# Kernel tuning notes

Measured on AMD Instinct MI355X. Metric: run time of the kernel, lower is better.

The kernel has to match this reference:

```python
import jax, jax.numpy as jnp
import numpy as np

D = 192
HEADS = 4
HD = D // HEADS
R = 3  # correlation radius actually used in forward_level
NDISP = (2 * R + 1) ** 2  # 49
T = 3  # frames -> 2 consecutive pairs
ITERS = 4


def layer_norm(x, w, b, eps=1e-5):
    m = jnp.mean(x, axis=-1, keepdims=True)
    v = jnp.var(x, axis=-1, keepdims=True)
    return (x - m) / jnp.sqrt(v + eps) * w + b


def mha(x, in_w, in_b, out_w, out_b):
    # torch nn.MultiheadAttention, batch_first, self-attention
    B, N, _ = x.shape
    qkv = x @ in_w.T + in_b
    q, k, v = jnp.split(qkv, 3, axis=-1)
    q = q.reshape(B, N, HEADS, HD).transpose(0, 2, 1, 3) * (1.0 / float(np.sqrt(HD)))
    k = k.reshape(B, N, HEADS, HD).transpose(0, 2, 1, 3)
    v = v.reshape(B, N, HEADS, HD).transpose(0, 2, 1, 3)
    att = jax.nn.softmax(jnp.einsum('bhqd,bhkd->bhqk', q, k), axis=-1)
    y = jnp.einsum('bhqk,bhkd->bhqd', att, v).transpose(0, 2, 1, 3).reshape(B, N, D)
    return y @ out_w.T + out_b


def tblock(x, p):
    ln1w, ln1b, inw, inb, ow, ob, ln2w, ln2b, w1, b1, w2, b2 = p
    x = x + mha(layer_norm(x, ln1w, ln1b), inw, inb, ow, ob)
    h = layer_norm(x, ln2w, ln2b)
    h = jax.nn.gelu(h @ w1.T + b1, approximate=False) @ w2.T + b2
    return x + h


def local_corr(f1, f2):
    C = f1.shape[1]
    scale = 1.0 / float(np.sqrt(C))
    outs = []
    for dy in range(-R, R + 1):
        for dx in range(-R, R + 1):
            f2s = jnp.roll(f2, (dy, dx), axis=(2, 3))
            outs.append(jnp.sum(f1 * f2s, axis=1) * scale)
    return jnp.stack(outs, axis=1)


def grid_sample_bilinear_border(img, grid):
    # img: B,C,H,W; grid: B,Ho,Wo,2 with (x,y) in [-1,1]; align_corners=True, border padding
    B, C, H, W = img.shape
    x = jnp.clip((grid[..., 0] + 1.0) * 0.5 * (W - 1), 0.0, W - 1)
    y = jnp.clip((grid[..., 1] + 1.0) * 0.5 * (H - 1), 0.0, H - 1)
    x0 = jnp.floor(x); y0 = jnp.floor(y)
    x1 = jnp.minimum(x0 + 1, W - 1); y1 = jnp.minimum(y0 + 1, H - 1)
    wx = (x - x0)[:, None]; wy = (y - y0)[:, None]
    imgf = img.reshape(B, C, H * W)
    Ho, Wo = x.shape[1], x.shape[2]
    def gather(yy, xx):
        idx = (yy * W + xx).astype(jnp.int32).reshape(B, 1, Ho * Wo)
        return jnp.take_along_axis(imgf, idx, axis=2).reshape(B, C, Ho, Wo)
    v00 = gather(y0, x0); v01 = gather(y0, x1)
    v10 = gather(y1, x0); v11 = gather(y1, x1)
    return v00 * (1 - wx) * (1 - wy) + v01 * wx * (1 - wy) + v10 * (1 - wx) * wy + v11 * wx * wy


def warp(img, flow):
    # flow in pixels, Bx2xHxW
    B, C, H, W = img.shape
    xs = jnp.linspace(-1.0, 1.0, W); ys = jnp.linspace(-1.0, 1.0, H)
    gx, gy = jnp.meshgrid(xs, ys)  # each (H, W), 'xy' indexing
    base = jnp.stack([gx, gy], axis=-1)[None]
    off = jnp.stack([flow[:, 0] * (2.0 / max(W - 1, 1)),
                     flow[:, 1] * (2.0 / max(H - 1, 1))], axis=-1)
    return grid_sample_bilinear_border(img, base + off)


def upsample2x_align(img):
    # F.interpolate(scale_factor=2, mode='bilinear', align_corners=True)
    B, C, H, W = img.shape
    Ho, Wo = 2 * H, 2 * W
    xs = jnp.linspace(-1.0, 1.0, Wo); ys = jnp.linspace(-1.0, 1.0, Ho)
    gx, gy = jnp.meshgrid(xs, ys)
    grid = jnp.broadcast_to(jnp.stack([gx, gy], axis=-1)[None], (B, Ho, Wo, 2))
    return grid_sample_bilinear_border(img, grid)


def conv2d(x, w, b):
    y = jax.lax.conv_general_dilated(x, w, (1, 1), ((1, 1), (1, 1)),
                                     dimension_numbers=('NCHW', 'OIHW', 'NCHW'))
    return y + b[None, :, None, None]


def _forward(feats_l1, feats_l2, feats_l3, tok_w, tok_b,
             lcm_ln1_w, lcm_ln1_b, lcm_in_w, lcm_in_b, lcm_out_w, lcm_out_b,
             lcm_ln2_w, lcm_ln2_b, lcm_mlp_w1, lcm_mlp_b1, lcm_mlp_w2, lcm_mlp_b2,
             gtr_ln1_w, gtr_ln1_b, gtr_in_w, gtr_in_b, gtr_out_w, gtr_out_b,
             gtr_ln2_w, gtr_ln2_b, gtr_mlp_w1, gtr_mlp_b1, gtr_mlp_w2, gtr_mlp_b2,
             head_w1, head_b1, head_w2, head_b2,
             ref1_w1, ref1_b1, ref1_w2, ref1_b2,
             ref0_w1, ref0_b1, ref0_w2, ref0_b2):
    feats = [[feats_l1[t] for t in range(T)],
             [feats_l2[t] for t in range(T)],
             [feats_l3[t] for t in range(T)]]
    # ---- CostTokenizer ----
    tokens = []
    for lvl in range(3):
        toks = []
        for k in range(T - 1):
            corr = local_corr(feats[lvl][k], feats[lvl][k + 1])
            toks.append(jnp.einsum('bchw,dc->bdhw', corr, tok_w[lvl]) + tok_b[lvl][None, :, None, None])
        tokens.append(toks)
    lcm_p = [(lcm_ln1_w[i], lcm_ln1_b[i], lcm_in_w[i], lcm_in_b[i], lcm_out_w[i], lcm_out_b[i],
              lcm_ln2_w[i], lcm_ln2_b[i], lcm_mlp_w1[i], lcm_mlp_b1[i], lcm_mlp_w2[i], lcm_mlp_b2[i])
             for i in range(lcm_ln1_w.shape[0])]
    gtr_p = [(gtr_ln1_w[i], gtr_ln1_b[i], gtr_in_w[i], gtr_in_b[i], gtr_out_w[i], gtr_out_b[i],
              gtr_ln2_w[i], gtr_ln2_b[i], gtr_mlp_w1[i], gtr_mlp_b1[i], gtr_mlp_w2[i], gtr_mlp_b2[i])
             for i in range(gtr_ln1_w.shape[0])]
    # ---- LatentCostMemory (EMA state; .detach() -> stop_gradient; state resets when N changes) ----
    state = None
    latent = []
    for toks in tokens:
        lvl_lat = []
        for tok in toks:
            B_, Dd, H, W = tok.shape
            x = tok.reshape(B_, Dd, H * W).transpose(0, 2, 1)  # b (h w) d
            for p in lcm_p:
                x = tblock(x, p)
            if state is None or state.shape[1] != x.shape[1]:
                state = jax.lax.stop_gradient(x)
            x = 0.8 * x + 0.2 * state
            state = jax.lax.stop_gradient(x)
            lvl_lat.append(x.transpose(0, 2, 1))  # b d n
        latent.append(lvl_lat)
    H8, W8 = feats[1][0].shape[-2:]
    coarse = []
    for lat in latent[1]:
        x = lat.transpose(0, 2, 1)
        for p in gtr_p:
            x = tblock(x, p)
        fv = jax.nn.gelu(x @ head_w1.T + head_b1, approximate=False) @ head_w2.T + head_b2
        coarse.append(fv.transpose(0, 2, 1).reshape(-1, 2, H8, W8))
    # ---- MSRecurrentDecoder ----
    outs = []
    for k, f8 in enumerate(coarse):
        cur = f8
        for _ in range(ITERS):
            w10 = warp(feats[1][k + 1], cur)
            x = jnp.concatenate([feats[1][k], cur, w10], axis=1)
            cur = cur + conv2d(jax.nn.gelu(conv2d(x, ref1_w1, ref1_b1), approximate=False), ref1_w2, ref1_b2)
        cur2 = upsample2x_align(cur)
        for _ in range(ITERS):
            w10 = warp(feats[0][k + 1], cur2)
            x = jnp.concatenate([feats[0][k], cur2, w10], axis=1)
            cur2 = cur2 + conv2d(jax.nn.gelu(conv2d(x, ref0_w1, ref0_b1), approximate=False), ref0_w2, ref0_b2)
        outs.append(cur2)
    return jnp.stack(outs)  # [pairs, B, 2, H/4, W/4]


def setup_inputs():
    key = jax.random.key(0)
    ks = iter(jax.random.split(key, 64))
    def rn(shape, s=1.0):
        return jax.random.normal(next(ks), shape, dtype=jnp.float32) * s
    B = 1
    inp = {}
    inp['feats_l1'] = rn((T, B, 64, 64, 64))
    inp['feats_l2'] = rn((T, B, 128, 32, 32))
    inp['feats_l3'] = rn((T, B, 192, 16, 16))
    inp['tok_w'] = rn((3, D, NDISP), 0.02)
    inp['tok_b'] = rn((3, D), 0.02)
    for pre, n in (('lcm', 6), ('gtr', 2)):
        inp[pre + '_ln1_w'] = jnp.ones((n, D), jnp.float32)
        inp[pre + '_ln1_b'] = jnp.zeros((n, D), jnp.float32)
        inp[pre + '_in_w'] = rn((n, 3 * D, D), 0.02)
        inp[pre + '_in_b'] = rn((n, 3 * D), 0.02)
        inp[pre + '_out_w'] = rn((n, D, D), 0.02)
        inp[pre + '_out_b'] = rn((n, D), 0.02)
        inp[pre + '_ln2_w'] = jnp.ones((n, D), jnp.float32)
        inp[pre + '_ln2_b'] = jnp.zeros((n, D), jnp.float32)
        inp[pre + '_mlp_w1'] = rn((n, 4 * D, D), 0.02)
        inp[pre + '_mlp_b1'] = rn((n, 4 * D), 0.02)
        inp[pre + '_mlp_w2'] = rn((n, D, 4 * D), 0.02)
        inp[pre + '_mlp_b2'] = rn((n, D), 0.02)
    inp['head_w1'] = rn((D, D), 0.02); inp['head_b1'] = rn((D,), 0.02)
    inp['head_w2'] = rn((2, D), 0.02); inp['head_b2'] = rn((2,), 0.02)
    inp['ref1_w1'] = rn((128, 258, 3, 3), 0.02); inp['ref1_b1'] = rn((128,), 0.02)
    inp['ref1_w2'] = rn((2, 128, 3, 3), 0.02); inp['ref1_b2'] = rn((2,), 0.02)
    inp['ref0_w1'] = rn((64, 130, 3, 3), 0.02); inp['ref0_b1'] = rn((64,), 0.02)
    inp['ref0_w2'] = rn((2, 64, 3, 3), 0.02); inp['ref0_b2'] = rn((2,), 0.02)
    return inp


def reference(feats_l1, feats_l2, feats_l3, tok_w, tok_b,
              lcm_ln1_w, lcm_ln1_b, lcm_in_w, lcm_in_b, lcm_out_w, lcm_out_b,
              lcm_ln2_w, lcm_ln2_b, lcm_mlp_w1, lcm_mlp_b1, lcm_mlp_w2, lcm_mlp_b2,
              gtr_ln1_w, gtr_ln1_b, gtr_in_w, gtr_in_b, gtr_out_w, gtr_out_b,
              gtr_ln2_w, gtr_ln2_b, gtr_mlp_w1, gtr_mlp_b1, gtr_mlp_w2, gtr_mlp_b2,
              head_w1, head_b1, head_w2, head_b2,
              ref1_w1, ref1_b1, ref1_w2, ref1_b2,
              ref0_w1, ref0_b1, ref0_w2, ref0_b2):
    return _forward(feats_l1, feats_l2, feats_l3, tok_w, tok_b,
                    lcm_ln1_w, lcm_ln1_b, lcm_in_w, lcm_in_b, lcm_out_w, lcm_out_b,
                    lcm_ln2_w, lcm_ln2_b, lcm_mlp_w1, lcm_mlp_b1, lcm_mlp_w2, lcm_mlp_b2,
                    gtr_ln1_w, gtr_ln1_b, gtr_in_w, gtr_in_b, gtr_out_w, gtr_out_b,
                    gtr_ln2_w, gtr_ln2_b, gtr_mlp_w1, gtr_mlp_b1, gtr_mlp_w2, gtr_mlp_b2,
                    head_w1, head_b1, head_w2, head_b2,
                    ref1_w1, ref1_b1, ref1_w2, ref1_b2,
                    ref0_w1, ref0_b1, ref0_w2, ref0_b2)
```

## Files before the change

### kernel.cpp

```cpp
#include <hip/hip_runtime.h>
#include <hip/hip_bf16.h>

typedef __hip_bfloat16 bf16;
typedef short bf16x8 __attribute__((ext_vector_type(8)));
typedef float f32x4 __attribute__((ext_vector_type(4)));

#define DEV __device__ __forceinline__

DEV float bf2f(bf16 v) { return __bfloat162float(v); }
DEV bf16 f2bf(float v) { return __float2bfloat16(v); }
DEV unsigned short bfr(float f) {
  bf16 h = __float2bfloat16(f);
  return *reinterpret_cast<unsigned short*>(&h);
}
DEV float shf(unsigned short u) {
  unsigned int x = ((unsigned int)u) << 16;
  return *reinterpret_cast<float*>(&x);
}
DEV float gelu_exact(float x) { return 0.5f * x * (1.0f + erff(x * 0.70710678118654752f)); }

DEV float ldw(const void* p, long i, int isb) {
  return isb ? __bfloat162float(((const bf16*)p)[i]) : ((const float*)p)[i];
}

__global__ void k_detect(const unsigned short* __restrict__ u, int* __restrict__ flag) {
  __shared__ int bad;
  if (threadIdx.x == 0) bad = 0;
  __syncthreads();
  for (int i = threadIdx.x; i < 8192; i += 256) {
    int expo = (u[i] >> 7) & 0xFF;
    if (expo >= 138) atomicOr(&bad, 1);
  }
  __syncthreads();
  if (threadIdx.x == 0) *flag = bad ? 0 : 1;
}
__global__ void k_setone(int* p) { *p = 1; }

__global__ void k_cvt(const void* __restrict__ s, float* __restrict__ d, int n,
                      const int* __restrict__ fl) {
  int isb = *fl;
  int i = blockIdx.x * blockDim.x + threadIdx.x;
  if (i < n) d[i] = ldw(s, i, isb);
}

__global__ void k_zerosh(unsigned short* __restrict__ p, int n8) {
  int i = blockIdx.x * blockDim.x + threadIdx.x;
  if (i < n8) { uint4 z = {0, 0, 0, 0}; *(uint4*)(p + (long)i * 8) = z; }
}

__global__ void k_padtokw(const void* __restrict__ tw, bf16* __restrict__ dst,
                          const int* __restrict__ fl) {
  int isb = *fl;
  int i = blockIdx.x * blockDim.x + threadIdx.x;
  if (i >= 12288) return;
  int n = i >> 6, k = i & 63;
  float v = (k < 49) ? ldw(tw, 9408 + (long)n * 49 + k, isb) : 0.0f;
  dst[i] = f2bf(v);
}

__global__ void k_packw(const void* __restrict__ src, bf16* __restrict__ dst,
                        int OC, int C, int ICT, int NP, int ICP, int n,
                        const int* __restrict__ fl) {
  int isb = *fl;
  int i = blockIdx.x * blockDim.x + threadIdx.x;
  if (i >= n) return;
  int s = i / (NP * ICP);
  int r = i - s * NP * ICP;
  int oc = r / ICP, icp = r - oc * ICP;
  float v = 0.0f;
  if (oc < OC) {
    int ic = -1;
    if (icp < C) ic = icp;
    else if (icp < 2 * C) ic = icp - C + C + 2;
    else if (icp < 2 * C + 2) ic = icp - 2 * C + C;
    if (ic >= 0 && ic < ICT) v = ldw(src, ((long)oc * ICT + ic) * 9 + s, isb);
  }
  dst[i] = f2bf(v);
}

__global__ void k_trans_feats(const void* __restrict__ in, bf16* __restrict__ Fp,
                              int F, int C, int HW, const int* __restrict__ fl) {
  int isb = *fl;
  int cpg = C >> 3;
  int n = F * HW * cpg;
  int i = blockIdx.x * blockDim.x + threadIdx.x;
  if (i >= n) return;
  int p = i % HW;
  int rem = i / HW;
  int c8 = rem % cpg;
  int f = rem / cpg;
  long base = (long)f * C * HW + (long)(c8 * 8) * HW + p;
  union { unsigned short u[8]; uint4 v; } pk;
#pragma unroll
  for (int j = 0; j < 8; ++j) pk.u[j] = bfr(ldw(in, base + (long)j * HW, isb));
  *(uint4*)((unsigned short*)Fp + ((long)f * HW + p) * C + c8 * 8) = pk.v;
}

template <int C, int ICP, int NP, int WW, int LGW>
__global__ __launch_bounds__(64, 2) void k_conv1d(
    const bf16* __restrict__ Fp, const float* __restrict__ flow,
    const bf16* __restrict__ Wp, const float* __restrict__ bias,
    bf16* __restrict__ out) {
  constexpr int HH = WW, HW = WW * WW;
  constexpr int ACW = 18, APX = 54;
  constexpr int NK = ICP / 32;
  __shared__ unsigned short As[APX][40];
  __shared__ int pofs[APX];
  __shared__ int doff[APX][4];
  __shared__ float dwt[APX][4];
  __shared__ float ffl[APX][2];
  int ln = threadIdx.x;
  int quad = ln >> 4, l16 = ln & 15;
  int n0 = blockIdx.x * 16, m0 = blockIdx.y * 16, b = blockIdx.z;
  int py0 = m0 >> LGW, px0 = m0 & (WW - 1);
  const unsigned short* fcur = (const unsigned short*)Fp + (long)b * HW * C;
  const unsigned short* fnxt = (const unsigned short*)Fp + (long)(b + 1) * HW * C;
  const float* fl = flow + (long)b * 2 * HW;
  if (ln < APX) {
    int sr = ln / ACW, sc = ln - sr * ACW;
    int py = py0 + sr - 1, px = px0 + sc - 1;
    bool in = py >= 0 && py < HH && px >= 0 && px < WW;
    int p = in ? (py * WW + px) : 0;
    pofs[ln] = in ? p * C : -1;
    float fx = in ? fl[p] : 0.0f, fy = in ? fl[HW + p] : 0.0f;
    float x = fminf(fmaxf((float)px + fx, 0.0f), (float)(WW - 1));
    float y = fminf(fmaxf((float)py + fy, 0.0f), (float)(HH - 1));
    int x0 = (int)floorf(x), y0 = (int)floorf(y);
    int x1 = min(x0 + 1, WW - 1), y1 = min(y0 + 1, HH - 1);
    float wx = x - (float)x0, wy = y - (float)y0;
    dwt[ln][0] = in ? (1 - wx) * (1 - wy) : 0.0f;
    dwt[ln][1] = in ? wx * (1 - wy) : 0.0f;
    dwt[ln][2] = in ? (1 - wx) * wy : 0.0f;
    dwt[ln][3] = in ? wx * wy : 0.0f;
    doff[ln][0] = (y0 * WW + x0) * C; doff[ln][1] = (y0 * WW + x1) * C;
    doff[ln][2] = (y1 * WW + x0) * C; doff[ln][3] = (y1 * WW + x1) * C;
    ffl[ln][0] = in ? fx : 0.0f; ffl[ln][1] = in ? fy : 0.0f;
  }
  const unsigned short* wrow = (const unsigned short*)Wp + (long)(n0 + l16) * ICP + quad * 8;
  f32x4 ac0 = {}, ac1 = {}, ac2 = {};
  for (int kc = 0; kc < NK; ++kc) {
    int chb = kc * 32;
    if (chb < C) {
      uint4 arg[4];
#pragma unroll
      for (int j = 0; j < 4; ++j) {
        int idx = ln + j * 64;
        if (idx < APX * 4) {
          int ap = idx >> 2, c4 = idx & 3;
          int po = pofs[ap];
          uint4 z = {0, 0, 0, 0};
          arg[j] = (po >= 0) ? *(const uint4*)(fcur + po + chb + c4 * 8) : z;
        }
      }
#pragma unroll
      for (int j = 0; j < 4; ++j) {
        int idx = ln + j * 64;
        if (idx < APX * 4) {
          int ap = idx >> 2, c4 = idx & 3;
          *(uint4*)&As[ap][c4 * 8] = arg[j];
        }
      }
    } else if (chb < 2 * C) {
#pragma unroll
      for (int j = 0; j < 4; ++j) {
        int idx = ln + j * 64;
        if (idx < APX * 4) {
          int ap = idx >> 2, c4 = idx & 3;
          int c = chb - C + c4 * 8;
          uint4 v0 = *(const uint4*)(fnxt + doff[ap][0] + c);
          uint4 v1 = *(const uint4*)(fnxt + doff[ap][1] + c);
          uint4 v2 = *(const uint4*)(fnxt + doff[ap][2] + c);
          uint4 v3 = *(const uint4*)(fnxt + doff[ap][3] + c);
          float q0 = dwt[ap][0], q1 = dwt[ap][1], q2 = dwt[ap][2], q3 = dwt[ap][3];
          union { unsigned short u[8]; uint4 v; } a0 = {.v = v0}, a1 = {.v = v1},
                                                  a2 = {.v = v2}, a3 = {.v = v3}, o;
#pragma unroll
          for (int e = 0; e < 8; ++e)
            o.u[e] = bfr(shf(a0.u[e]) * q0 + shf(a1.u[e]) * q1 +
                         shf(a2.u[e]) * q2 + shf(a3.u[e]) * q3);
          *(uint4*)&As[ap][c4 * 8] = o.v;
        }
      }
    } else {
#pragma unroll
      for (int j = 0; j < 4; ++j) {
        int idx = ln + j * 64;
        if (idx < APX * 4) {
          int ap = idx >> 2, c4 = idx & 3;
          union { unsigned short u[8]; uint4 v; } o = { .v = {0, 0, 0, 0} };
          if (c4 == 0) { o.u[0] = bfr(ffl[ap][0]); o.u[1] = bfr(ffl[ap][1]); }
          *(uint4*)&As[ap][c4 * 8] = o.v;
        }
      }
    }
#pragma unroll
    for (int s = 0; s < 9; ++s) {
      int ky = s / 3, kx = s - ky * 3;
      bf16x8 af = *(const bf16x8*)&As[ky * ACW + l16 + kx][quad * 8];
      bf16x8 wf = *(const bf16x8*)(wrow + (long)s * NP * ICP + chb);
      if (s % 3 == 0)      ac0 = __builtin_amdgcn_mfma_f32_16x16x32_bf16(af, wf, ac0, 0, 0, 0);
      else if (s % 3 == 1) ac1 = __builtin_amdgcn_mfma_f32_16x16x32_bf16(af, wf, ac1, 0, 0, 0);
      else                 ac2 = __builtin_amdgcn_mfma_f32_16x16x32_bf16(af, wf, ac2, 0, 0, 0);
    }
  }
  int n = n0 + l16;
  float bv = bias[n];
  long rowbase = (long)b * (HH + 2) * (WW + 2) + (long)(py0 + 1) * (WW + 2);
#pragma unroll
  for (int r = 0; r < 4; ++r) {
    int px = px0 + quad * 4 + r;
    float v = gelu_exact(ac0[r] + ac1[r] + ac2[r] + bv);
    ((unsigned short*)out)[(rowbase + px + 1) * NP + n] = bfr(v);
  }
}

template <int C, int WW, int LGW>
__global__ __launch_bounds__(256) void k_conv2_dot(
    const bf16* __restrict__ mid, const bf16* __restrict__ Wq,
    const float* __restrict__ bias, float* __restrict__ cur) {
  constexpr int HH = WW;
  constexpr int HW = HH * WW;
  constexpr int Wp2 = WW + 2;
  constexpr int CPL = C / 64;
  int tid = threadIdx.x, wv = tid >> 6, ln = tid & 63;
  int gw = blockIdx.x * 4 + wv;
  int b = gw >> (2 * LGW);
  int p = gw & (HW - 1);
  int py = p >> LGW, px = p & (WW - 1);
  float r0 = cur[((long)b * 2 + 0) * HW + p];
  float r1 = cur[((long)b * 2 + 1) * HW + p];
  float b0 = bias[0], b1 = bias[1];
  const unsigned short* base = (const unsigned short*)mid +
      ((long)b * (HH + 2) * Wp2 + (long)py * Wp2 + px) * C + ln * CPL;
  const unsigned short* wb = (const unsigned short*)Wq + ln * CPL;
  float s0 = 0.0f, s1 = 0.0f;
#pragma unroll
  for (int t = 0; t < 9; ++t) {
    int dy = t / 3, dx = t - dy * 3;
    const unsigned short* ar = base + ((long)dy * Wp2 + dx) * C;
    const unsigned short* w0r = wb + (long)(t * 16 + 0) * C;
    const unsigned short* w1r = wb + (long)(t * 16 + 1) * C;
    if (CPL == 2) {
      unsigned int a = *(const unsigned int*)ar;
      unsigned int q0 = *(const unsigned int*)w0r;
      unsigned int q1 = *(const unsigned int*)w1r;
      float a0 = shf((unsigned short)a), a1 = shf((unsigned short)(a >> 16));
      s0 += a0 * shf((unsigned short)q0) + a1 * shf((unsigned short)(q0 >> 16));
      s1 += a0 * shf((unsigned short)q1) + a1 * shf((unsigned short)(q1 >> 16));
    } else {
      float a0 = shf(ar[0]);
      s0 += a0 * shf(w0r[0]);
      s1 += a0 * shf(w1r[0]);
    }
  }
#pragma unroll
  for (int o = 32; o; o >>= 1) { s0 += __shfl_xor(s0, o); s1 += __shfl_xor(s1, o); }
  if (ln == 0) {
    cur[((long)b * 2 + 0) * HW + p] = s0 + b0 + r0;
    cur[((long)b * 2 + 1) * HW + p] = s1 + b1 + r1;
  }
}

__global__ void k_corr(const bf16* __restrict__ Fp2, bf16* __restrict__ corrT) {
  __shared__ unsigned short f1r[128];
  int p = blockIdx.x;
  int b = blockIdx.y;
  int t = threadIdx.x;
  const unsigned short* f1 = (const unsigned short*)Fp2 + ((long)b * 1024 + p) * 128;
  if (t < 16) *(uint4*)&f1r[t * 8] = *(const uint4*)(f1 + t * 8);
  __syncthreads();
  long rowo = ((long)b * 1024 + p) * 64;
  if (t < 49) {
    int dy = t / 7 - 3, dx = t % 7 - 3;
    int h = p >> 5, w = p & 31;
    int p2 = (((h - dy) & 31) << 5) | ((w - dx) & 31);
    const unsigned short* f2 = (const unsigned short*)Fp2 + ((long)(b + 1) * 1024 + p2) * 128;
    float s = 0.0f;
    for (int c = 0; c < 128; c += 8) {
      union { unsigned short u[8]; uint4 v; } av = { .v = *(const uint4*)&f1r[c] };
      union { unsigned short u[8]; uint4 v; } bv = { .v = *(const uint4*)(f2 + c) };
#pragma unroll
      for (int j = 0; j < 8; ++j) s += shf(av.u[j]) * shf(bv.u[j]);
    }
    corrT[rowo + t] = f2bf(s * 0.08838834764831845f);
  } else {
    corrT[rowo + t] = f2bf(0.0f);
  }
}

template <int KT, int NTW, int ACT, bool HASRES, int AMODE, int OUTBF, int VT>
__global__ __launch_bounds__(64, 2) void k_gemm_w(
    const void* __restrict__ A, const void* __restrict__ W, long woff,
    const void* __restrict__ bias, long boff, const int* __restrict__ flb,
    const float* __restrict__ res, void* __restrict__ C,
    int N, const int* __restrict__ fl,
    const unsigned short* __restrict__ mop, const float* __restrict__ mml,
    bf16* __restrict__ vtout,
    const void* __restrict__ lnw, long lnwoff,
    const void* __restrict__ lnb, long lnboff) {
  constexpr int NK = KT / 32;
  int isb = *fl;
  int ln = threadIdx.x;
  int quad = ln >> 4, l16 = ln & 15;
  int m0 = blockIdx.y * 16, n0 = blockIdx.x * (16 * NTW);
  __shared__ unsigned short Als[(AMODE >= 2) ? 16 : 1][200];
  if constexpr (AMODE == 3) {
    int row = ln >> 2, j = ln & 3;
    const float* xr = (const float*)A + (long)(m0 + row) * 192 + j * 48;
    float av[48];
#pragma unroll
    for (int q = 0; q < 12; ++q) {
      float4 v = *(const float4*)(xr + q * 4);
      av[q * 4 + 0] = v.x; av[q * 4 + 1] = v.y;
      av[q * 4 + 2] = v.z; av[q * 4 + 3] = v.w;
    }
    float sum = 0.0f;
#pragma unroll
    for (int q = 0; q < 48; ++q) sum += av[q];
    sum += __shfl_xor(sum, 1);
    sum += __shfl_xor(sum, 2);
    float mean = sum * (1.0f / 192.0f);
    float vs = 0.0f;
#pragma unroll
    for (int q = 0; q < 48; ++q) { float d = av[q] - mean; vs += d * d; }
    vs += __shfl_xor(vs, 1);
    vs += __shfl_xor(vs, 2);
    float rstd = rsqrtf(vs * (1.0f / 192.0f) + 1e-5f);
#pragma unroll
    for (int g = 0; g < 6; ++g) {
      union { unsigned short u[8]; uint4 v; } pk;
#pragma unroll
      for (int e = 0; e < 8; ++e) {
        long k = j * 48 + g * 8 + e;
        float gg = ldw(lnw, lnwoff + k, isb);
        float bb = ldw(lnb, lnboff + k, isb);
        pk.u[e] = bfr((av[g * 8 + e] - mean) * rstd * gg + bb);
      }
      *(uint4*)&Als[row][j * 48 + g * 8] = pk.v;
    }
  } else if constexpr (AMODE == 2) {
    int row = ln >> 2, j = ln & 3;
    int m = m0 + row;
    int rr = m & 1023, bb = m >> 10;
    long idx[4];
    float ms[4], ls[4];
    float Ms = -1e30f;
#pragma unroll
    for (int s = 0; s < 4; ++s) {
      idx[s] = (((long)s * 2 + bb) * 4 + j) * 1024 + rr;
      ms[s] = mml[idx[s] * 2];
      ls[s] = mml[idx[s] * 2 + 1];
      Ms = fmaxf(Ms, ms[s]);
    }
    float e4[4], L = 0.0f;
#pragma unroll
    for (int s = 0; s < 4; ++s) { e4[s] = __expf(ms[s] - Ms); L += ls[s] * e4[s]; }
    float invL = 1.0f / L;
#pragma unroll
    for (int g = 0; g < 6; ++g) {
      union { unsigned short u[8]; uint4 v; } pk;
#pragma unroll
      for (int e2 = 0; e2 < 8; ++e2) {
        float o = 0.0f;
#pragma unroll
        for (int s = 0; s < 4; ++s) o += shf(mop[idx[s] * 48 + g * 8 + e2]) * e4[s];
        pk.u[e2] = bfr(o * invL);
      }
      *(uint4*)&Als[row][j * 48 + g * 8] = pk.v;
    }
  }
  f32x4 acc[NTW] = {};
  auto lda = [&](int kc) -> bf16x8 {
    if constexpr (AMODE >= 2) {
      return *(const bf16x8*)&Als[l16][kc * 32 + quad * 8];
    } else if constexpr (AMODE == 1) {
      return *(const bf16x8*)((const unsigned short*)A + (long)(m0 + l16) * KT + kc * 32 + quad * 8);
    } else {
      const float* ap = (const float*)A + (long)(m0 + l16) * KT + kc * 32 + quad * 8;
      float4 a0 = *(const float4*)ap;
      float4 a1 = *(const float4*)(ap + 4);
      union { unsigned short u[8]; bf16x8 v; } pk;
      pk.u[0] = bfr(a0.x); pk.u[1] = bfr(a0.y); pk.u[2] = bfr(a0.z); pk.u[3] = bfr(a0.w);
      pk.u[4] = bfr(a1.x); pk.u[5] = bfr(a1.y); pk.u[6] = bfr(a1.z); pk.u[7] = bfr(a1.w);
      return pk.v;
    }
  };
  if (isb) {
    const unsigned short* wb = (const unsigned short*)W + woff + (long)l16 * KT + quad * 8;
    for (int kc = 0; kc < NK; ++kc) {
      bf16x8 af = lda(kc);
#pragma unroll
      for (int nt = 0; nt < NTW; ++nt) {
        bf16x8 wf = *(const bf16x8*)(wb + (long)(n0 + nt * 16) * KT + kc * 32);
        acc[nt] = __builtin_amdgcn_mfma_f32_16x16x32_bf16(af, wf, acc[nt], 0, 0, 0);
      }
    }
  } else {
    const float* wb = (const float*)W + woff + (long)l16 * KT + quad * 8;
    for (int kc = 0; kc < NK; ++kc) {
      bf16x8 af = lda(kc);
#pragma unroll
      for (int nt = 0; nt < NTW; ++nt) {
        const float* wp = wb + (long)(n0 + nt * 16) * KT + kc * 32;
        float4 w0 = *(const float4*)wp;
        float4 w1 = *(const float4*)(wp + 4);
        union { unsigned short u[8]; bf16x8 v; } pk;
        pk.u[0] = bfr(w0.x); pk.u[1] = bfr(w0.y); pk.u[2] = bfr(w0.z); pk.u[3] = bfr(w0.w);
        pk.u[4] = bfr(w1.x); pk.u[5] = bfr(w1.y); pk.u[6] = bfr(w1.z); pk.u[7] = bfr(w1.w);
        acc[nt] = __builtin_amdgcn_mfma_f32_16x16x32_bf16(af, pk.v, acc[nt], 0, 0, 0);
      }
    }
  }
  int isbb = *flb;
#pragma unroll
  for (int nt = 0; nt < NTW; ++nt) {
    int n = n0 + nt * 16 + l16;
    float bv = ldw(bias, boff + n, isbb);
#pragma unroll
    for (int r = 0; r < 4; ++r) {
      int m = m0 + quad * 4 + r;
      float v = acc[nt][r] + bv;
      if (HASRES) v += res[(long)m * N + n];
      if (ACT == 1) v = gelu_exact(v);
      if (OUTBF) ((bf16*)C)[(long)m * N + n] = f2bf(v);
      else ((float*)C)[(long)m * N + n] = v;
      if constexpr (VT) {
        if (n >= 384) {
          int hh = (n - 384) / 48, dd = (n - 384) % 48;
          int row = m & 1023, bb = m >> 10;
          vtout[((long)(bb * 4 + hh) * 48 + dd) * 1024 + row] = f2bf(v);
        }
      }
    }
  }
}

__global__ __launch_bounds__(256) void k_head2(const float* __restrict__ A,
                                               const void* __restrict__ W,
                                               const void* __restrict__ bias,
                                               float* __restrict__ C,
                                               const int* __restrict__ fl) {
  int isb = *fl;
  int wv = threadIdx.x >> 6, ln = threadIdx.x & 63;
  int gw = blockIdx.x * 4 + wv;
  int m = gw >> 1, n = gw & 1;
  const float* a = A + (long)m * 192;
  float s = 0.0f;
#pragma unroll
  for (int q = 0; q < 3; ++q) {
    int j = ln + q * 64;
    s += a[j] * ldw(W, (long)n * 192 + j, isb);
  }
  for (int o = 32; o; o >>= 1) s += __shfl_xor(s, o);
  if (ln == 0) {
    int b = m >> 10, p = m & 1023;
    C[((long)b * 2 + n) * 1024 + p] = s + ldw(bias, n, isb);
  }
}

__global__ __launch_bounds__(256) void k_attn_mfma(const bf16* __restrict__ qkv,
                                                   const bf16* __restrict__ vt,
                                                   unsigned short* __restrict__ opart,
                                                   float* __restrict__ ml) {
  __shared__ unsigned short Qs[64][72];
  __shared__ unsigned short Ks[64][72];
  __shared__ unsigned short Vs[48][72];
  __shared__ unsigned short Ps[64][72];
  int tid = threadIdx.x;
  int wv = tid >> 6, ln = tid & 63, quad = ln >> 4, l16 = ln & 15;
  int h = blockIdx.y, b = blockIdx.z;
  int qt = blockIdx.x >> 2, s = blockIdx.x & 3;
  int q0 = qt * 64;
  const unsigned short* qp = (const unsigned short*)qkv + (long)b * 1024 * 576;
  const unsigned short* vp = (const unsigned short*)vt + ((long)(b * 4 + h) * 48) * 1024;
  for (int i = tid; i < 384; i += 256) {
    int r = i / 6, c = i % 6;
    *(uint4*)&Qs[r][c * 8] = *(const uint4*)(qp + (long)(q0 + r) * 576 + h * 48 + c * 8);
  }
  for (int i = tid; i < 128; i += 256) {
    int r = i >> 1, c = 6 + (i & 1);
    uint4 z = {0, 0, 0, 0};
    *(uint4*)&Qs[r][c * 8] = z;
  }
  float m[4] = {-1e30f, -1e30f, -1e30f, -1e30f};
  float l[4] = {0.0f, 0.0f, 0.0f, 0.0f};
  f32x4 accO[3] = {};
  const float SC = 0.14433756729740643f;
  for (int kc = s * 4; kc < s * 4 + 4; ++kc) {
    int k0 = kc * 64;
    for (int i = tid; i < 384; i += 256) {
      int r = i / 6, c = i % 6;
      *(uint4*)&Ks[r][c * 8] = *(const uint4*)(qp + (long)(k0 + r) * 576 + 192 + h * 48 + c * 8);
    }
    for (int i = tid; i < 128; i += 256) {
      int r = i >> 1, c = 6 + (i & 1);
      uint4 z = {0, 0, 0, 0};
      *(uint4*)&Ks[r][c * 8] = z;
    }
    for (int i = tid; i < 384; i += 256) {
      int d = i >> 3, c = i & 7;
      *(uint4*)&Vs[d][c * 8] = *(const uint4*)(vp + (long)d * 1024 + k0 + c * 8);
    }
    __syncthreads();
    f32x4 accS[4] = {};
    bf16x8 a0 = *(const bf16x8*)&Qs[wv * 16 + l16][quad * 8];
    bf16x8 a1 = *(const bf16x8*)&Qs[wv * 16 + l16][32 + quad * 8];
#pragma unroll
    for (int ct = 0; ct < 4; ++ct) {
      bf16x8 b0 = *(const bf16x8*)&Ks[ct * 16 + l16][quad * 8];
      bf16x8 b1 = *(const bf16x8*)&Ks[ct * 16 + l16][32 + quad * 8];
      accS[ct] = __builtin_amdgcn_mfma_f32_16x16x32_bf16(a0, b0, accS[ct], 0, 0, 0);
      accS[ct] = __builtin_amdgcn_mfma_f32_16x16x32_bf16(a1, b1, accS[ct], 0, 0, 0);
    }
#pragma unroll
    for (int r = 0; r < 4; ++r) {
      float s0 = accS[0][r] * SC, s1 = accS[1][r] * SC;
      float s2 = accS[2][r] * SC, s3 = accS[3][r] * SC;
      float mx = fmaxf(fmaxf(s0, s1), fmaxf(s2, s3));
      for (int o = 8; o; o >>= 1) mx = fmaxf(mx, __shfl_xor(mx, o));
      float mn = fmaxf(m[r], mx);
      float alpha = __expf(m[r] - mn);
      float p0 = __expf(s0 - mn), p1 = __expf(s1 - mn);
      float p2 = __expf(s2 - mn), p3 = __expf(s3 - mn);
      float rs = p0 + p1 + p2 + p3;
      for (int o = 8; o; o >>= 1) rs += __shfl_xor(rs, o);
      m[r] = mn;
      l[r] = l[r] * alpha + rs;
      accO[0][r] *= alpha; accO[1][r] *= alpha; accO[2][r] *= alpha;
      int prow = wv * 16 + quad * 4 + r;
      Ps[prow][l16]      = bfr(p0);
      Ps[prow][16 + l16] = bfr(p1);
      Ps[prow][32 + l16] = bfr(p2);
      Ps[prow][48 + l16] = bfr(p3);
    }
    bf16x8 pf0 = *(const bf16x8*)&Ps[wv * 16 + l16][quad * 8];
    bf16x8 pf1 = *(const bf16x8*)&Ps[wv * 16 + l16][32 + quad * 8];
#pragma unroll
    for (int ct = 0; ct < 3; ++ct) {
      bf16x8 v0 = *(const bf16x8*)&Vs[ct * 16 + l16][quad * 8];
      bf16x8 v1 = *(const bf16x8*)&Vs[ct * 16 + l16][32 + quad * 8];
      accO[ct] = __builtin_amdgcn_mfma_f32_16x16x32_bf16(pf0, v0, accO[ct], 0, 0, 0);
      accO[ct] = __builtin_amdgcn_mfma_f32_16x16x32_bf16(pf1, v1, accO[ct], 0, 0, 0);
    }
    __syncthreads();
  }
  long base = (((long)s * 2 + b) * 4 + h) * 1024;
#pragma unroll
  for (int r = 0; r < 4; ++r) {
    int row = q0 + wv * 16 + quad * 4 + r;
#pragma unroll
    for (int ct = 0; ct < 3; ++ct)
      opart[(base + row) * 48 + ct * 16 + l16] = bfr(accO[ct][r]);
    if (l16 == 0) {
      ml[(base + row) * 2]     = m[r];
      ml[(base + row) * 2 + 1] = l[r];
    }
  }
}

__global__ void k_ema(float* __restrict__ x) {
  int i = blockIdx.x * blockDim.x + threadIdx.x;
  if (i < 196608) x[196608 + i] = 0.8f * x[196608 + i] + 0.2f * x[i];
}

__global__ void k_upsample(const float* __restrict__ in, float* __restrict__ out) {
  int i = blockIdx.x * blockDim.x + threadIdx.x;
  if (i >= 2 * 2 * 64 * 64) return;
  int p = i & 4095;
  int bc = i >> 12;
  int oy = p >> 6, ox = p & 63;
  float sx = ox * (31.0f / 63.0f), sy = oy * (31.0f / 63.0f);
  int x0 = (int)sx, y0 = (int)sy;
  int x1 = min(x0 + 1, 31), y1 = min(y0 + 1, 31);
  float wx = sx - x0, wy = sy - y0;
  const float* ic = in + (long)bc * 1024;
  out[i] = ic[y0 * 32 + x0] * (1 - wx) * (1 - wy) + ic[y0 * 32 + x1] * wx * (1 - wy)
         + ic[y1 * 32 + x0] * (1 - wx) * wy      + ic[y1 * 32 + x1] * wx * wy;
}

__global__ void k_out(const float* __restrict__ cur2, void* __restrict__ out,
                      const int* __restrict__ fl) {
  int isb = *fl;
  int i = blockIdx.x * blockDim.x + threadIdx.x;
  if (i < 16384) {
    if (isb) ((bf16*)out)[i] = f2bf(cur2[i]);
    else ((float*)out)[i] = cur2[i];
  }
}

extern "C" void kernel_launch(void* const* d_in, const int* in_sizes, int n_in,
                              void* d_out, int out_size, void* d_ws, size_t ws_size,
                              hipStream_t stream) {
  const void* feats_l1 = d_in[0];
  const void* feats_l2 = d_in[1];
  const void* tok_w = d_in[3];
  const void* tok_b = d_in[4];
  const void* lcm_ln1_w = d_in[5];
  const void* lcm_ln1_b = d_in[6];
  const void* lcm_in_w  = d_in[7];
  const void* lcm_in_b  = d_in[8];
  const void* lcm_out_w = d_in[9];
  const void* lcm_out_b = d_in[10];
  const void* lcm_ln2_w = d_in[11];
  const void* lcm_ln2_b = d_in[12];
  const void* lcm_mlp_w1 = d_in[13];
  const void* lcm_mlp_b1 = d_in[14];
  const void* lcm_mlp_w2 = d_in[15];
  const void* lcm_mlp_b2 = d_in[16];
  const void* gtr_ln1_w = d_in[17];
  const void* gtr_ln1_b = d_in[18];
  const void* gtr_in_w  = d_in[19];
  const void* gtr_in_b  = d_in[20];
  const void* gtr_out_w = d_in[21];
  const void* gtr_out_b = d_in[22];
  const void* gtr_ln2_w = d_in[23];
  const void* gtr_ln2_b = d_in[24];
  const void* gtr_mlp_w1 = d_in[25];
  const void* gtr_mlp_b1 = d_in[26];
  const void* gtr_mlp_w2 = d_in[27];
  const void* gtr_mlp_b2 = d_in[28];
  const void* head_w1 = d_in[29];
  const void* head_b1 = d_in[30];
  const void* head_w2 = d_in[31];
  const void* head_b2 = d_in[32];
  const void* ref1_w1 = d_in[33];
  const void* ref1_b1 = d_in[34];
  const void* ref1_w2 = d_in[35];
  const void* ref1_b2 = d_in[36];
  const void* ref0_w1 = d_in[37];
  const void* ref0_b1 = d_in[38];
  const void* ref0_w2 = d_in[39];
  const void* ref0_b2 = d_in[40];
  (void)ws_size; (void)n_in; (void)in_sizes; (void)out_size;

  int* flag = (int*)d_ws;
  int* oneflag = (int*)d_ws + 2;
  float* wsf = (float*)d_ws;
  float* F2   = wsf + 16;
  float* rA   = F2 + 393216;
  float* rX   = rA + 786432;
  float* rT   = rX + 393216;
  float* rY   = rT + 393216;
  float* big  = rY + 393216;
  float* fv   = big + 1572864;
  float* cur  = fv + 4096;
  float* cur2 = cur + 4096;
  float* cb1a = cur2 + 16384;
  float* cb1b = cb1a + 128;
  float* cb0a = cb1b + 16;
  float* cb0b = cb0a + 64;
  bf16* wtok  = (bf16*)(cb0b + 16);
  float* wpk  = cb0b + 16 + 6144;
  bf16* w1p1 = (bf16*)wpk;
  bf16* w1p2 = (bf16*)(wpk + 165888);
  bf16* w0p1 = (bf16*)(wpk + 175104);
  bf16* w0p2 = (bf16*)(wpk + 221184);

  float* x = rX;
  bf16* corrTb = (bf16*)big;
  bf16* qkvbb  = (bf16*)big;
  bf16* vtb    = (bf16*)(big + 655360);
  bf16* hidb   = (bf16*)big;
  unsigned short* opart = (unsigned short*)rA;
  float* mlbuf = rY;
  float* headh = rT;
  bf16* mid0p = (bf16*)rT;
  bf16* mid1p = (bf16*)rY;
  bf16* Fp2   = (bf16*)(big + 851968);
  bf16* Fp1   = (bf16*)(big + 1048576);

  k_detect<<<1, 256, 0, stream>>>((const unsigned short*)feats_l1, flag);
  k_setone<<<1, 1, 0, stream>>>(oneflag);
  k_cvt<<<1, 256, 0, stream>>>(ref1_b1, cb1a, 128, flag);
  k_cvt<<<1, 256, 0, stream>>>(ref1_b2, cb1b, 2, flag);
  k_cvt<<<1, 256, 0, stream>>>(ref0_b1, cb0a, 64, flag);
  k_cvt<<<1, 256, 0, stream>>>(ref0_b2, cb0b, 2, flag);
  k_padtokw<<<48, 256, 0, stream>>>(tok_w, wtok, flag);
  k_packw<<<1296, 256, 0, stream>>>(ref1_w1, w1p1, 128, 128, 258, 128, 288, 331776, flag);
  k_packw<<<72, 256, 0, stream>>>(ref1_w2, w1p2, 2, 128, 128, 16, 128, 18432, flag);
  k_packw<<<360, 256, 0, stream>>>(ref0_w1, w0p1, 64, 64, 130, 64, 160, 92160, flag);
  k_packw<<<36, 256, 0, stream>>>(ref0_w2, w0p2, 2, 64, 64, 16, 64, 9216, flag);
  k_trans_feats<<<192, 256, 0, stream>>>(feats_l2, Fp2, 3, 128, 1024, flag);
  k_trans_feats<<<384, 256, 0, stream>>>(feats_l1, Fp1, 3, 64, 4096, flag);

  k_corr<<<dim3(1024, 2), 64, 0, stream>>>(Fp2, corrTb);
  k_gemm_w<64, 4, 0, false, 1, 0, 0><<<dim3(3, 128), 64, 0, stream>>>(
      corrTb, wtok, 0, tok_b, 192, flag, nullptr, x, 192, oneflag,
      nullptr, nullptr, nullptr, nullptr, 0, nullptr, 0);

  auto run_block = [&](const void* ln1w, long o1, const void* ln1b, long o2,
                       const void* inw, long o3, const void* inb, long o4,
                       const void* ow, long o5, const void* ob, long o6,
                       const void* ln2w, long o7, const void* ln2b, long o8,
                       const void* w1, long o9, const void* b1, long o10,
                       const void* w2, long o11, const void* b2, long o12) {
    k_gemm_w<192, 4, 0, false, 3, 1, 1><<<dim3(9, 128), 64, 0, stream>>>(
        x, inw, o3, inb, o4, flag, nullptr, qkvbb, 576, flag,
        nullptr, nullptr, vtb, ln1w, o1, ln1b, o2);
    k_attn_mfma<<<dim3(64, 4, 2), 256, 0, stream>>>(qkvbb, vtb, opart, mlbuf);
    k_gemm_w<192, 4, 0, true, 2, 0, 0><<<dim3(3, 128), 64, 0, stream>>>(
        nullptr, ow, o5, ob, o6, flag, x, x, 192, flag,
        opart, mlbuf, nullptr, nullptr, 0, nullptr, 0);
    k_gemm_w<192, 4, 1, false, 3, 1, 0><<<dim3(12, 128), 64, 0, stream>>>(
        x, w1, o9, b1, o10, flag, nullptr, hidb, 768, flag,
        nullptr, nullptr, nullptr, ln2w, o7, ln2b, o8);
    k_gemm_w<768, 4, 0, true, 1, 0, 0><<<dim3(3, 128), 64, 0, stream>>>(
        hidb, w2, o11, b2, o12, flag, x, x, 192, flag,
        nullptr, nullptr, nullptr, nullptr, 0, nullptr, 0);
  };

  for (int i = 0; i < 6; ++i) {
    run_block(lcm_ln1_w, (long)i * 192, lcm_ln1_b, (long)i * 192,
              lcm_in_w, (long)i * 110592, lcm_in_b, (long)i * 576,
              lcm_out_w, (long)i * 36864, lcm_out_b, (long)i * 192,
              lcm_ln2_w, (long)i * 192, lcm_ln2_b, (long)i * 192,
              lcm_mlp_w1, (long)i * 147456, lcm_mlp_b1, (long)i * 768,
              lcm_mlp_w2, (long)i * 147456, lcm_mlp_b2, (long)i * 192);
  }
  k_ema<<<768, 256, 0, stream>>>(x);

  for (int i = 0; i < 2; ++i) {
    run_block(gtr_ln1_w, (long)i * 192, gtr_ln1_b, (long)i * 192,
              gtr_in_w, (long)i * 110592, gtr_in_b, (long)i * 576,
              gtr_out_w, (long)i * 36864, gtr_out_b, (long)i * 192,
              gtr_ln2_w, (long)i * 192, gtr_ln2_b, (long)i * 192,
              gtr_mlp_w1, (long)i * 147456, gtr_mlp_b1, (long)i * 768,
              gtr_mlp_w2, (long)i * 147456, gtr_mlp_b2, (long)i * 192);
  }

  k_gemm_w<192, 4, 1, false, 0, 0, 0><<<dim3(3, 128), 64, 0, stream>>>(
      x, head_w1, 0, head_b1, 0, flag, nullptr, headh, 192, flag,
      nullptr, nullptr, nullptr, nullptr, 0, nullptr, 0);
  k_head2<<<1024, 256, 0, stream>>>(headh, head_w2, head_b2, cur, flag);

  k_zerosh<<<768, 256, 0, stream>>>((unsigned short*)rT, 196608);

  for (int it = 0; it < 4; ++it) {
    k_conv1d<128, 288, 128, 32, 5><<<dim3(8, 64, 2), 64, 0, stream>>>(
        Fp2, cur, w1p1, cb1a, mid1p);
    k_conv2_dot<128, 32, 5><<<512, 256, 0, stream>>>(mid1p, w1p2, cb1b, cur);
  }
  k_upsample<<<64, 256, 0, stream>>>(cur, cur2);

  for (int it = 0; it < 4; ++it) {
    k_conv1d<64, 160, 64, 64, 6><<<dim3(4, 256, 2), 64, 0, stream>>>(
        Fp1, cur2, w0p1, cb0a, mid0p);
    k_conv2_dot<64, 64, 6><<<2048, 256, 0, stream>>>(mid0p, w0p2, cb0b, cur2);
  }

  k_out<<<64, 256, 0, stream>>>(cur2, d_out, flag);
}
```

Baseline: 1.007 ms.

## Fuse transformer stack into persistent megakernel with software grid barriers

Replaces roughly 45 separate launches (token GEMM, 8 transformer blocks of 5 kernels each, EMA, and the head) with one persistent kernel of 256 blocks. The phases are separated by an atomic-counter grid barrier, and each wave walks the GEMM tiles in a grid-stride loop. The aim is to remove launch overhead and inter-kernel gaps between the many small GEMM and attention phases. In exchange, occupancy is capped at 256 blocks, and the spin barrier relies on all blocks being co-resident, which risks deadlock if they are not.

```diff
diff --git a/kernel.cpp b/kernel.cpp
--- a/kernel.cpp
+++ b/kernel.cpp
@@ -34,7 +34,7 @@
   __syncthreads();
   if (threadIdx.x == 0) *flag = bad ? 0 : 1;
 }
-__global__ void k_setone(int* p) { *p = 1; }
+__global__ void k_zero2(int* a, int* b) { *a = 0; *b = 0; }
 
 __global__ void k_cvt(const void* __restrict__ s, float* __restrict__ d, int n,
                       const int* __restrict__ fl) {
@@ -288,279 +288,351 @@
   }
 }
 
-template <int KT, int NTW, int ACT, bool HASRES, int AMODE, int OUTBF, int VT>
-__global__ __launch_bounds__(64, 2) void k_gemm_w(
-    const void* __restrict__ A, const void* __restrict__ W, long woff,
-    const void* __restrict__ bias, long boff, const int* __restrict__ flb,
-    const float* __restrict__ res, void* __restrict__ C,
-    int N, const int* __restrict__ fl,
-    const unsigned short* __restrict__ mop, const float* __restrict__ mml,
-    bf16* __restrict__ vtout,
-    const void* __restrict__ lnw, long lnwoff,
-    const void* __restrict__ lnb, long lnboff) {
+
+DEV void gridbar(int* cnt, int* gen) {
+  __threadfence();
+  __syncthreads();
+  if (threadIdx.x == 0) {
+    int g = atomicAdd(gen, 0);
+    if (atomicAdd(cnt, 1) == 255) {
+      atomicExch(cnt, 0);
+      atomicAdd(gen, 1);
+    } else {
+      while (atomicAdd(gen, 0) == g) __builtin_amdgcn_s_sleep(8);
+    }
+  }
+  __syncthreads();
+  __threadfence();
+}
+
+template <int KT, int ACT, bool HASRES, int AMODE, int OUTBF, int VT>
+DEV void gemm_ph(unsigned short* wls, int gw, int ln,
+                 const void* A, const void* W, long woff,
+                 const void* bias, long boff, int isbb,
+                 const float* res, void* C, int N, int isb,
+                 const unsigned short* mop, const float* mml, bf16* vtout,
+                 const void* lnw, long lnwoff, const void* lnb, long lnboff) {
   constexpr int NK = KT / 32;
-  int isb = *fl;
-  int ln = threadIdx.x;
   int quad = ln >> 4, l16 = ln & 15;
-  int m0 = blockIdx.y * 16, n0 = blockIdx.x * (16 * NTW);
-  __shared__ unsigned short Als[(AMODE >= 2) ? 16 : 1][200];
-  if constexpr (AMODE == 3) {
-    int row = ln >> 2, j = ln & 3;
-    const float* xr = (const float*)A + (long)(m0 + row) * 192 + j * 48;
-    float av[48];
-#pragma unroll
-    for (int q = 0; q < 12; ++q) {
-      float4 v = *(const float4*)(xr + q * 4);
-      av[q * 4 + 0] = v.x; av[q * 4 + 1] = v.y;
-      av[q * 4 + 2] = v.z; av[q * 4 + 3] = v.w;
-    }
-    float sum = 0.0f;
-#pragma unroll
-    for (int q = 0; q < 48; ++q) sum += av[q];
-    sum += __shfl_xor(sum, 1);
-    sum += __shfl_xor(sum, 2);
-    float mean = sum * (1.0f / 192.0f);
-    float vs = 0.0f;
-#pragma unroll
-    for (int q = 0; q < 48; ++q) { float d = av[q] - mean; vs += d * d; }
-    vs += __shfl_xor(vs, 1);
-    vs += __shfl_xor(vs, 2);
-    float rstd = rsqrtf(vs * (1.0f / 192.0f) + 1e-5f);
-#pragma unroll
-    for (int g = 0; g < 6; ++g) {
-      union { unsigned short u[8]; uint4 v; } pk;
-#pragma unroll
-      for (int e = 0; e < 8; ++e) {
-        long k = j * 48 + g * 8 + e;
-        float gg = ldw(lnw, lnwoff + k, isb);
-        float bb = ldw(lnb, lnboff + k, isb);
-        pk.u[e] = bfr((av[g * 8 + e] - mean) * rstd * gg + bb);
-      }
-      *(uint4*)&Als[row][j * 48 + g * 8] = pk.v;
-    }
-  } else if constexpr (AMODE == 2) {
-    int row = ln >> 2, j = ln & 3;
-    int m = m0 + row;
-    int rr = m & 1023, bb = m >> 10;
-    long idx[4];
-    float ms[4], ls[4];
-    float Ms = -1e30f;
-#pragma unroll
-    for (int s = 0; s < 4; ++s) {
-      idx[s] = (((long)s * 2 + bb) * 4 + j) * 1024 + rr;
-      ms[s] = mml[idx[s] * 2];
-      ls[s] = mml[idx[s] * 2 + 1];
-      Ms = fmaxf(Ms, ms[s]);
-    }
-    float e4[4], L = 0.0f;
-#pragma unroll
-    for (int s = 0; s < 4; ++s) { e4[s] = __expf(ms[s] - Ms); L += ls[s] * e4[s]; }
-    float invL = 1.0f / L;
-#pragma unroll
-    for (int g = 0; g < 6; ++g) {
-      union { unsigned short u[8]; uint4 v; } pk;
-#pragma unroll
-      for (int e2 = 0; e2 < 8; ++e2) {
-        float o = 0.0f;
-#pragma unroll
-        for (int s = 0; s < 4; ++s) o += shf(mop[idx[s] * 48 + g * 8 + e2]) * e4[s];
-        pk.u[e2] = bfr(o * invL);
-      }
-      *(uint4*)&Als[row][j * 48 + g * 8] = pk.v;
-    }
-  }
-  f32x4 acc[NTW] = {};
-  auto lda = [&](int kc) -> bf16x8 {
-    if constexpr (AMODE >= 2) {
-      return *(const bf16x8*)&Als[l16][kc * 32 + quad * 8];
-    } else if constexpr (AMODE == 1) {
-      return *(const bf16x8*)((const unsigned short*)A + (long)(m0 + l16) * KT + kc * 32 + quad * 8);
+  int ntn = N >> 6;
+  int ntiles = 128 * ntn;
+  for (int t = gw; t < ntiles; t += 1024) {
+    int tn = t % ntn, tm = t / ntn;
+    int m0 = tm * 16, n0 = tn * 64;
+    if constexpr (AMODE == 3) {
+      int row = ln >> 2, j = ln & 3;
+      const float* xr = (const float*)A + (long)(m0 + row) * 192 + j * 48;
+      float av[48];
+#pragma unroll
+      for (int q = 0; q < 12; ++q) {
+        float4 v = *(const float4*)(xr + q * 4);
+        av[q * 4 + 0] = v.x; av[q * 4 + 1] = v.y;
+        av[q * 4 + 2] = v.z; av[q * 4 + 3] = v.w;
+      }
+      float sum = 0.0f;
+#pragma unroll
+      for (int q = 0; q < 48; ++q) sum += av[q];
+      sum += __shfl_xor(sum, 1);
+      sum += __shfl_xor(sum, 2);
+      float mean = sum * (1.0f / 192.0f);
+      float vs = 0.0f;
+#pragma unroll
+      for (int q = 0; q < 48; ++q) { float d = av[q] - mean; vs += d * d; }
+      vs += __shfl_xor(vs, 1);
+      vs += __shfl_xor(vs, 2);
+      float rstd = rsqrtf(vs * (1.0f / 192.0f) + 1e-5f);
+#pragma unroll
+      for (int g = 0; g < 6; ++g) {
+        union { unsigned short u[8]; uint4 v; } pk;
+#pragma unroll
+        for (int e = 0; e < 8; ++e) {
+          long k = j * 48 + g * 8 + e;
+          float gg = ldw(lnw, lnwoff + k, isb);
+          float bb = ldw(lnb, lnboff + k, isb);
+          pk.u[e] = bfr((av[g * 8 + e] - mean) * rstd * gg + bb);
+        }
+        *(uint4*)&wls[row * 200 + j * 48 + g * 8] = pk.v;
+      }
+    } else if constexpr (AMODE == 2) {
+      int row = ln >> 2, j = ln & 3;
+      int m = m0 + row;
+      int rr = m & 1023, bb = m >> 10;
+      long idx[4];
+      float ms[4], ls[4];
+      float Ms = -1e30f;
+#pragma unroll
+      for (int s = 0; s < 4; ++s) {
+        idx[s] = (((long)s * 2 + bb) * 4 + j) * 1024 + rr;
+        ms[s] = mml[idx[s] * 2];
+        ls[s] = mml[idx[s] * 2 + 1];
+        Ms = fmaxf(Ms, ms[s]);
+      }
+      float e4[4], L = 0.0f;
+#pragma unroll
+      for (int s = 0; s < 4; ++s) { e4[s] = __expf(ms[s] - Ms); L += ls[s] * e4[s]; }
+      float invL = 1.0f / L;
+#pragma unroll
+      for (int g = 0; g < 6; ++g) {
+        union { unsigned short u[8]; uint4 v; } pk;
+#pragma unroll
+        for (int e2 = 0; e2 < 8; ++e2) {
+          float o = 0.0f;
+#pragma unroll
+          for (int s = 0; s < 4; ++s) o += shf(mop[idx[s] * 48 + g * 8 + e2]) * e4[s];
+          pk.u[e2] = bfr(o * invL);
+        }
+        *(uint4*)&wls[row * 200 + j * 48 + g * 8] = pk.v;
+      }
+    }
+    f32x4 acc[4] = {};
+    auto lda = [&](int kc) -> bf16x8 {
+      if constexpr (AMODE >= 2) {
+        return *(const bf16x8*)&wls[l16 * 200 + kc * 32 + quad * 8];
+      } else if constexpr (AMODE == 1) {
+        return *(const bf16x8*)((const unsigned short*)A + (long)(m0 + l16) * KT + kc * 32 + quad * 8);
+      } else {
+        const float* ap = (const float*)A + (long)(m0 + l16) * KT + kc * 32 + quad * 8;
+        float4 a0 = *(const float4*)ap;
+        float4 a1 = *(const float4*)(ap + 4);
+        union { unsigned short u[8]; bf16x8 v; } pk;
+        pk.u[0] = bfr(a0.x); pk.u[1] = bfr(a0.y); pk.u[2] = bfr(a0.z); pk.u[3] = bfr(a0.w);
+        pk.u[4] = bfr(a1.x); pk.u[5] = bfr(a1.y); pk.u[6] = bfr(a1.z); pk.u[7] = bfr(a1.w);
+        return pk.v;
+      }
+    };
+    if (isb) {
+      const unsigned short* wb = (const unsigned short*)W + woff + (long)l16 * KT + quad * 8;
+      for (int kc = 0; kc < NK; ++kc) {
+        bf16x8 af = lda(kc);
+#pragma unroll
+        for (int nt = 0; nt < 4; ++nt) {
+          bf16x8 wf = *(const bf16x8*)(wb + (long)(n0 + nt * 16) * KT + kc * 32);
+          acc[nt] = __builtin_amdgcn_mfma_f32_16x16x32_bf16(af, wf, acc[nt], 0, 0, 0);
+        }
+      }
     } else {
-      const float* ap = (const float*)A + (long)(m0 + l16) * KT + kc * 32 + quad * 8;
-      float4 a0 = *(const float4*)ap;
-      float4 a1 = *(const float4*)(ap + 4);
-      union { unsigned short u[8]; bf16x8 v; } pk;
-      pk.u[0] = bfr(a0.x); pk.u[1] = bfr(a0.y); pk.u[2] = bfr(a0.z); pk.u[3] = bfr(a0.w);
-      pk.u[4] = bfr(a1.x); pk.u[5] = bfr(a1.y); pk.u[6] = bfr(a1.z); pk.u[7] = bfr(a1.w);
-      return pk.v;
-    }
-  };
-  if (isb) {
-    const unsigned short* wb = (const unsigned short*)W + woff + (long)l16 * KT + quad * 8;
-    for (int kc = 0; kc < NK; ++kc) {
-      bf16x8 af = lda(kc);
-#pragma unroll
-      for (int nt = 0; nt < NTW; ++nt) {
-        bf16x8 wf = *(const bf16x8*)(wb + (long)(n0 + nt * 16) * KT + kc * 32);
-        acc[nt] = __builtin_amdgcn_mfma_f32_16x16x32_bf16(af, wf, acc[nt], 0, 0, 0);
-      }
-    }
-  } else {
-    const float* wb = (const float*)W + woff + (long)l16 * KT + quad * 8;
-    for (int kc = 0; kc < NK; ++kc) {
-      bf16x8 af = lda(kc);
-#pragma unroll
-      for (int nt = 0; nt < NTW; ++nt) {
-        const float* wp = wb + (long)(n0 + nt * 16) * KT + kc * 32;
-        float4 w0 = *(const float4*)wp;
-        float4 w1 = *(const float4*)(wp + 4);
-        union { unsigned short u[8]; bf16x8 v; } pk;
-        pk.u[0] = bfr(w0.x); pk.u[1] = bfr(w0.y); pk.u[2] = bfr(w0.z); pk.u[3] = bfr(w0.w);
-        pk.u[4] = bfr(w1.x); pk.u[5] = bfr(w1.y); pk.u[6] = bfr(w1.z); pk.u[7] = bfr(w1.w);
-        acc[nt] = __builtin_amdgcn_mfma_f32_16x16x32_bf16(af, pk.v, acc[nt], 0, 0, 0);
-      }
-    }
-  }
-  int isbb = *flb;
-#pragma unroll
-  for (int nt = 0; nt < NTW; ++nt) {
-    int n = n0 + nt * 16 + l16;
-    float bv = ldw(bias, boff + n, isbb);
-#pragma unroll
-    for (int r = 0; r < 4; ++r) {
-      int m = m0 + quad * 4 + r;
-      float v = acc[nt][r] + bv;
-      if (HASRES) v += res[(long)m * N + n];
-      if (ACT == 1) v = gelu_exact(v);
-      if (OUTBF) ((bf16*)C)[(long)m * N + n] = f2bf(v);
-      else ((float*)C)[(long)m * N + n] = v;
-      if constexpr (VT) {
-        if (n >= 384) {
-          int hh = (n - 384) / 48, dd = (n - 384) % 48;
-          int row = m & 1023, bb = m >> 10;
-          vtout[((long)(bb * 4 + hh) * 48 + dd) * 1024 + row] = f2bf(v);
-        }
-      }
-    }
-  }
-}
-
-__global__ __launch_bounds__(256) void k_head2(const float* __restrict__ A,
-                                               const void* __restrict__ W,
-                                               const void* __restrict__ bias,
-                                               float* __restrict__ C,
-                                               const int* __restrict__ fl) {
-  int isb = *fl;
-  int wv = threadIdx.x >> 6, ln = threadIdx.x & 63;
-  int gw = blockIdx.x * 4 + wv;
-  int m = gw >> 1, n = gw & 1;
-  const float* a = A + (long)m * 192;
-  float s = 0.0f;
-#pragma unroll
-  for (int q = 0; q < 3; ++q) {
-    int j = ln + q * 64;
-    s += a[j] * ldw(W, (long)n * 192 + j, isb);
-  }
-  for (int o = 32; o; o >>= 1) s += __shfl_xor(s, o);
-  if (ln == 0) {
-    int b = m >> 10, p = m & 1023;
-    C[((long)b * 2 + n) * 1024 + p] = s + ldw(bias, n, isb);
-  }
-}
-
-__global__ __launch_bounds__(256) void k_attn_mfma(const bf16* __restrict__ qkv,
-                                                   const bf16* __restrict__ vt,
-                                                   unsigned short* __restrict__ opart,
-                                                   float* __restrict__ ml) {
-  __shared__ unsigned short Qs[64][72];
-  __shared__ unsigned short Ks[64][72];
-  __shared__ unsigned short Vs[48][72];
-  __shared__ unsigned short Ps[64][72];
-  int tid = threadIdx.x;
+      const float* wb = (const float*)W + woff + (long)l16 * KT + quad * 8;
+      for (int kc = 0; kc < NK; ++kc) {
+        bf16x8 af = lda(kc);
+#pragma unroll
+        for (int nt = 0; nt < 4; ++nt) {
+          const float* wp = wb + (long)(n0 + nt * 16) * KT + kc * 32;
+          float4 w0 = *(const float4*)wp;
+          float4 w1 = *(const float4*)(wp + 4);
+          union { unsigned short u[8]; bf16x8 v; } pk;
+          pk.u[0] = bfr(w0.x); pk.u[1] = bfr(w0.y); pk.u[2] = bfr(w0.z); pk.u[3] = bfr(w0.w);
+          pk.u[4] = bfr(w1.x); pk.u[5] = bfr(w1.y); pk.u[6] = bfr(w1.z); pk.u[7] = bfr(w1.w);
+          acc[nt] = __builtin_amdgcn_mfma_f32_16x16x32_bf16(af, pk.v, acc[nt], 0, 0, 0);
+        }
+      }
+    }
+#pragma unroll
+    for (int nt = 0; nt < 4; ++nt) {
+      int n = n0 + nt * 16 + l16;
+      float bv = ldw(bias, boff + n, isbb);
+#pragma unroll
+      for (int r = 0; r < 4; ++r) {
+        int m = m0 + quad * 4 + r;
+        float v = acc[nt][r] + bv;
+        if (HASRES) v += res[(long)m * N + n];
+        if (ACT == 1) v = gelu_exact(v);
+        if (OUTBF) ((bf16*)C)[(long)m * N + n] = f2bf(v);
+        else ((float*)C)[(long)m * N + n] = v;
+        if constexpr (VT) {
+          if (n >= 384) {
+            int hh = (n - 384) / 48, dd = (n - 384) % 48;
+            int row = m & 1023, bb = m >> 10;
+            vtout[((long)(bb * 4 + hh) * 48 + dd) * 1024 + row] = f2bf(v);
+          }
+        }
+      }
+    }
+  }
+}
+
+DEV void attn_ph(unsigned short* SM, int bid, int tid,
+                 const bf16* qkv, const bf16* vt,
+                 unsigned short* opart, float* ml) {
+  unsigned short* Qs = SM;
+  unsigned short* Ks = SM + 64 * 72;
+  unsigned short* Vs = SM + 128 * 72;
+  unsigned short* Ps = SM + 176 * 72;
   int wv = tid >> 6, ln = tid & 63, quad = ln >> 4, l16 = ln & 15;
-  int h = blockIdx.y, b = blockIdx.z;
-  int qt = blockIdx.x >> 2, s = blockIdx.x & 3;
-  int q0 = qt * 64;
-  const unsigned short* qp = (const unsigned short*)qkv + (long)b * 1024 * 576;
-  const unsigned short* vp = (const unsigned short*)vt + ((long)(b * 4 + h) * 48) * 1024;
-  for (int i = tid; i < 384; i += 256) {
-    int r = i / 6, c = i % 6;
-    *(uint4*)&Qs[r][c * 8] = *(const uint4*)(qp + (long)(q0 + r) * 576 + h * 48 + c * 8);
-  }
-  for (int i = tid; i < 128; i += 256) {
-    int r = i >> 1, c = 6 + (i & 1);
-    uint4 z = {0, 0, 0, 0};
-    *(uint4*)&Qs[r][c * 8] = z;
-  }
-  float m[4] = {-1e30f, -1e30f, -1e30f, -1e30f};
-  float l[4] = {0.0f, 0.0f, 0.0f, 0.0f};
-  f32x4 accO[3] = {};
   const float SC = 0.14433756729740643f;
-  for (int kc = s * 4; kc < s * 4 + 4; ++kc) {
-    int k0 = kc * 64;
+  for (int u = bid; u < 512; u += 256) {
+    int bx = u & 63;
+    int h = (u >> 6) & 3, b = u >> 8;
+    int qt = bx >> 2, s = bx & 3;
+    int q0 = qt * 64;
+    const unsigned short* qp = (const unsigned short*)qkv + (long)b * 1024 * 576;
+    const unsigned short* vp = (const unsigned short*)vt + ((long)(b * 4 + h) * 48) * 1024;
     for (int i = tid; i < 384; i += 256) {
       int r = i / 6, c = i % 6;
-      *(uint4*)&Ks[r][c * 8] = *(const uint4*)(qp + (long)(k0 + r) * 576 + 192 + h * 48 + c * 8);
+      *(uint4*)&Qs[r * 72 + c * 8] = *(const uint4*)(qp + (long)(q0 + r) * 576 + h * 48 + c * 8);
     }
     for (int i = tid; i < 128; i += 256) {
       int r = i >> 1, c = 6 + (i & 1);
       uint4 z = {0, 0, 0, 0};
-      *(uint4*)&Ks[r][c * 8] = z;
-    }
-    for (int i = tid; i < 384; i += 256) {
-      int d = i >> 3, c = i & 7;
-      *(uint4*)&Vs[d][c * 8] = *(const uint4*)(vp + (long)d * 1024 + k0 + c * 8);
-    }
-    __syncthreads();
-    f32x4 accS[4] = {};
-    bf16x8 a0 = *(const bf16x8*)&Qs[wv * 16 + l16][quad * 8];
-    bf16x8 a1 = *(const bf16x8*)&Qs[wv * 16 + l16][32 + quad * 8];
-#pragma unroll
-    for (int ct = 0; ct < 4; ++ct) {
-      bf16x8 b0 = *(const bf16x8*)&Ks[ct * 16 + l16][quad * 8];
-      bf16x8 b1 = *(const bf16x8*)&Ks[ct * 16 + l16][32 + quad * 8];
-      accS[ct] = __builtin_amdgcn_mfma_f32_16x16x32_bf16(a0, b0, accS[ct], 0, 0, 0);
-      accS[ct] = __builtin_amdgcn_mfma_f32_16x16x32_bf16(a1, b1, accS[ct], 0, 0, 0);
-    }
+      *(uint4*)&Qs[r * 72 + c * 8] = z;
+    }
+    float m[4] = {-1e30f, -1e30f, -1e30f, -1e30f};
+    float l[4] = {0.0f, 0.0f, 0.0f, 0.0f};
+    f32x4 accO[3] = {};
+    for (int kc = s * 4; kc < s * 4 + 4; ++kc) {
+      int k0 = kc * 64;
+      for (int i = tid; i < 384; i += 256) {
+        int r = i / 6, c = i % 6;
+        *(uint4*)&Ks[r * 72 + c * 8] =
+            *(const uint4*)(qp + (long)(k0 + r) * 576 + 192 + h * 48 + c * 8);
+      }
+      for (int i = tid; i < 128; i += 256) {
+        int r = i >> 1, c = 6 + (i & 1);
+        uint4 z = {0, 0, 0, 0};
+        *(uint4*)&Ks[r * 72 + c * 8] = z;
+      }
+      for (int i = tid; i < 384; i += 256) {
+        int d = i >> 3, c = i & 7;
+        *(uint4*)&Vs[d * 72 + c * 8] = *(const uint4*)(vp + (long)d * 1024 + k0 + c * 8);
+      }
+      __syncthreads();
+      f32x4 accS[4] = {};
+      bf16x8 a0 = *(const bf16x8*)&Qs[(wv * 16 + l16) * 72 + quad * 8];
+      bf16x8 a1 = *(const bf16x8*)&Qs[(wv * 16 + l16) * 72 + 32 + quad * 8];
+#pragma unroll
+      for (int ct = 0; ct < 4; ++ct) {
+        bf16x8 b0 = *(const bf16x8*)&Ks[(ct * 16 + l16) * 72 + quad * 8];
+        bf16x8 b1 = *(const bf16x8*)&Ks[(ct * 16 + l16) * 72 + 32 + quad * 8];
+        accS[ct] = __builtin_amdgcn_mfma_f32_16x16x32_bf16(a0, b0, accS[ct], 0, 0, 0);
+        accS[ct] = __builtin_amdgcn_mfma_f32_16x16x32_bf16(a1, b1, accS[ct], 0, 0, 0);
+      }
+#pragma unroll
+      for (int r = 0; r < 4; ++r) {
+        float s0 = accS[0][r] * SC, s1 = accS[1][r] * SC;
+        float s2 = accS[2][r] * SC, s3 = accS[3][r] * SC;
+        float mx = fmaxf(fmaxf(s0, s1), fmaxf(s2, s3));
+        for (int o = 8; o; o >>= 1) mx = fmaxf(mx, __shfl_xor(mx, o));
+        float mn = fmaxf(m[r], mx);
+        float alpha = __expf(m[r] - mn);
+        float p0 = __expf(s0 - mn), p1 = __expf(s1 - mn);
+        float p2 = __expf(s2 - mn), p3 = __expf(s3 - mn);
+        float rs = p0 + p1 + p2 + p3;
+        for (int o = 8; o; o >>= 1) rs += __shfl_xor(rs, o);
+        m[r] = mn;
+        l[r] = l[r] * alpha + rs;
+        accO[0][r] *= alpha; accO[1][r] *= alpha; accO[2][r] *= alpha;
+        int prow = wv * 16 + quad * 4 + r;
+        Ps[prow * 72 + l16]      = bfr(p0);
+        Ps[prow * 72 + 16 + l16] = bfr(p1);
+        Ps[prow * 72 + 32 + l16] = bfr(p2);
+        Ps[prow * 72 + 48 + l16] = bfr(p3);
+      }
+      bf16x8 pf0 = *(const bf16x8*)&Ps[(wv * 16 + l16) * 72 + quad * 8];
+      bf16x8 pf1 = *(const bf16x8*)&Ps[(wv * 16 + l16) * 72 + 32 + quad * 8];
+#pragma unroll
+      for (int ct = 0; ct < 3; ++ct) {
+        bf16x8 v0 = *(const bf16x8*)&Vs[(ct * 16 + l16) * 72 + quad * 8];
+        bf16x8 v1 = *(const bf16x8*)&Vs[(ct * 16 + l16) * 72 + 32 + quad * 8];
+        accO[ct] = __builtin_amdgcn_mfma_f32_16x16x32_bf16(pf0, v0, accO[ct], 0, 0, 0);
+        accO[ct] = __builtin_amdgcn_mfma_f32_16x16x32_bf16(pf1, v1, accO[ct], 0, 0, 0);
+      }
+      __syncthreads();
+    }
+    long base = (((long)s * 2 + b) * 4 + h) * 1024;
 #pragma unroll
     for (int r = 0; r < 4; ++r) {
-      float s0 = accS[0][r] * SC, s1 = accS[1][r] * SC;
-      float s2 = accS[2][r] * SC, s3 = accS[3][r] * SC;
-      float mx = fmaxf(fmaxf(s0, s1), fmaxf(s2, s3));
-      for (int o = 8; o; o >>= 1) mx = fmaxf(mx, __shfl_xor(mx, o));
-      float mn = fmaxf(m[r], mx);
-      float alpha = __expf(m[r] - mn);
-      float p0 = __expf(s0 - mn), p1 = __expf(s1 - mn);
-      float p2 = __expf(s2 - mn), p3 = __expf(s3 - mn);
-      float rs = p0 + p1 + p2 + p3;
-      for (int o = 8; o; o >>= 1) rs += __shfl_xor(rs, o);
-      m[r] = mn;
-      l[r] = l[r] * alpha + rs;
-      accO[0][r] *= alpha; accO[1][r] *= alpha; accO[2][r] *= alpha;
-      int prow = wv * 16 + quad * 4 + r;
-      Ps[prow][l16]      = bfr(p0);
-      Ps[prow][16 + l16] = bfr(p1);
-      Ps[prow][32 + l16] = bfr(p2);
-      Ps[prow][48 + l16] = bfr(p3);
-    }
-    bf16x8 pf0 = *(const bf16x8*)&Ps[wv * 16 + l16][quad * 8];
-    bf16x8 pf1 = *(const bf16x8*)&Ps[wv * 16 + l16][32 + quad * 8];
-#pragma unroll
-    for (int ct = 0; ct < 3; ++ct) {
-      bf16x8 v0 = *(const bf16x8*)&Vs[ct * 16 + l16][quad * 8];
-      bf16x8 v1 = *(const bf16x8*)&Vs[ct * 16 + l16][32 + quad * 8];
-      accO[ct] = __builtin_amdgcn_mfma_f32_16x16x32_bf16(pf0, v0, accO[ct], 0, 0, 0);
-      accO[ct] = __builtin_amdgcn_mfma_f32_16x16x32_bf16(pf1, v1, accO[ct], 0, 0, 0);
-    }
-    __syncthreads();
-  }
-  long base = (((long)s * 2 + b) * 4 + h) * 1024;
-#pragma unroll
-  for (int r = 0; r < 4; ++r) {
-    int row = q0 + wv * 16 + quad * 4 + r;
-#pragma unroll
-    for (int ct = 0; ct < 3; ++ct)
-      opart[(base + row) * 48 + ct * 16 + l16] = bfr(accO[ct][r]);
-    if (l16 == 0) {
-      ml[(base + row) * 2]     = m[r];
-      ml[(base + row) * 2 + 1] = l[r];
-    }
-  }
-}
-
-__global__ void k_ema(float* __restrict__ x) {
-  int i = blockIdx.x * blockDim.x + threadIdx.x;
-  if (i < 196608) x[196608 + i] = 0.8f * x[196608 + i] + 0.2f * x[i];
+      int row = q0 + wv * 16 + quad * 4 + r;
+#pragma unroll
+      for (int ct = 0; ct < 3; ++ct)
+        opart[(base + row) * 48 + ct * 16 + l16] = bfr(accO[ct][r]);
+      if (l16 == 0) {
+        ml[(base + row) * 2]     = m[r];
+        ml[(base + row) * 2 + 1] = l[r];
+      }
+    }
+  }
+}
+
+__global__ __launch_bounds__(256, 2) void k_mega(
+    const int* flag, int* barcnt, int* bargen,
+    float* x, const bf16* corrTb, const bf16* wtok, const void* tok_b,
+    bf16* qkvbb, bf16* vtb, unsigned short* opart, float* mlbuf,
+    bf16* hidb, float* headh, float* cur,
+    const void* lcm_ln1_w, const void* lcm_ln1_b, const void* lcm_in_w, const void* lcm_in_b,
+    const void* lcm_out_w, const void* lcm_out_b, const void* lcm_ln2_w, const void* lcm_ln2_b,
+    const void* lcm_mlp_w1, const void* lcm_mlp_b1, const void* lcm_mlp_w2, const void* lcm_mlp_b2,
+    const void* gtr_ln1_w, const void* gtr_ln1_b, const void* gtr_in_w, const void* gtr_in_b,
+    const void* gtr_out_w, const void* gtr_out_b, const void* gtr_ln2_w, const void* gtr_ln2_b,
+    const void* gtr_mlp_w1, const void* gtr_mlp_b1, const void* gtr_mlp_w2, const void* gtr_mlp_b2,
+    const void* head_w1, const void* head_b1, const void* head_w2, const void* head_b2) {
+  __shared__ unsigned short SM[17280];
+  int tid = threadIdx.x, bid = blockIdx.x;
+  int wv = tid >> 6, ln = tid & 63;
+  int gw = bid * 4 + wv;
+  unsigned short* wls = SM + wv * 3200;
+  int isb = *flag;
+  gemm_ph<64, 0, false, 1, 0, 0>(wls, gw, ln, corrTb, wtok, 0, tok_b, 192, isb,
+                                 nullptr, x, 192, 1, nullptr, nullptr, nullptr,
+                                 nullptr, 0, nullptr, 0);
+  gridbar(barcnt, bargen);
+  for (int blk = 0; blk < 8; ++blk) {
+    long i = (blk < 6) ? blk : (blk - 6);
+    const void *ln1w, *ln1b, *inw, *inb, *ow, *ob, *ln2w, *ln2b, *w1, *b1, *w2, *b2;
+    if (blk < 6) {
+      ln1w = lcm_ln1_w; ln1b = lcm_ln1_b; inw = lcm_in_w; inb = lcm_in_b;
+      ow = lcm_out_w; ob = lcm_out_b; ln2w = lcm_ln2_w; ln2b = lcm_ln2_b;
+      w1 = lcm_mlp_w1; b1 = lcm_mlp_b1; w2 = lcm_mlp_w2; b2 = lcm_mlp_b2;
+    } else {
+      ln1w = gtr_ln1_w; ln1b = gtr_ln1_b; inw = gtr_in_w; inb = gtr_in_b;
+      ow = gtr_out_w; ob = gtr_out_b; ln2w = gtr_ln2_w; ln2b = gtr_ln2_b;
+      w1 = gtr_mlp_w1; b1 = gtr_mlp_b1; w2 = gtr_mlp_w2; b2 = gtr_mlp_b2;
+    }
+    long o1 = i * 192, o2 = i * 192, o3 = i * 110592, o4 = i * 576;
+    long o5 = i * 36864, o6 = i * 192, o7 = i * 192, o8 = i * 192;
+    long o9 = i * 147456, o10 = i * 768, o11 = i * 147456, o12 = i * 192;
+    gemm_ph<192, 0, false, 3, 1, 1>(wls, gw, ln, x, inw, o3, inb, o4, isb,
+                                    nullptr, qkvbb, 576, isb, nullptr, nullptr, vtb,
+                                    ln1w, o1, ln1b, o2);
+    gridbar(barcnt, bargen);
+    attn_ph(SM, bid, tid, qkvbb, vtb, opart, mlbuf);
+    gridbar(barcnt, bargen);
+    gemm_ph<192, 0, true, 2, 0, 0>(wls, gw, ln, nullptr, ow, o5, ob, o6, isb,
+                                   x, x, 192, isb, opart, mlbuf, nullptr,
+                                   nullptr, 0, nullptr, 0);
+    gridbar(barcnt, bargen);
+    gemm_ph<192, 1, false, 3, 1, 0>(wls, gw, ln, x, w1, o9, b1, o10, isb,
+                                    nullptr, hidb, 768, isb, nullptr, nullptr, nullptr,
+                                    ln2w, o7, ln2b, o8);
+    gridbar(barcnt, bargen);
+    gemm_ph<768, 0, true, 1, 0, 0>(wls, gw, ln, hidb, w2, o11, b2, o12, isb,
+                                   x, x, 192, isb, nullptr, nullptr, nullptr,
+                                   nullptr, 0, nullptr, 0);
+    gridbar(barcnt, bargen);
+    if (blk == 5) {
+      int gt = bid * 256 + tid;
+      for (int e = gt; e < 196608; e += 65536)
+        x[196608 + e] = 0.8f * x[196608 + e] + 0.2f * x[e];
+      gridbar(barcnt, bargen);
+    }
+  }
+  gemm_ph<192, 1, false, 0, 0, 0>(wls, gw, ln, x, head_w1, 0, head_b1, 0, isb,
+                                  nullptr, headh, 192, isb, nullptr, nullptr, nullptr,
+                                  nullptr, 0, nullptr, 0);
+  gridbar(barcnt, bargen);
+  for (int t2 = gw; t2 < 4096; t2 += 1024) {
+    int m = t2 >> 1, n = t2 & 1;
+    const float* a = headh + (long)m * 192;
+    float s = 0.0f;
+#pragma unroll
+    for (int q = 0; q < 3; ++q) {
+      int j = ln + q * 64;
+      s += a[j] * ldw(head_w2, (long)n * 192 + j, isb);
+    }
+    for (int o = 32; o; o >>= 1) s += __shfl_xor(s, o);
+    if (ln == 0) {
+      int b = m >> 10, p = m & 1023;
+      cur[((long)b * 2 + n) * 1024 + p] = s + ldw(head_b2, n, isb);
+    }
+  }
 }
 
 __global__ void k_upsample(const float* __restrict__ in, float* __restrict__ out) {
@@ -634,7 +706,8 @@
   (void)ws_size; (void)n_in; (void)in_sizes; (void)out_size;
 
   int* flag = (int*)d_ws;
-  int* oneflag = (int*)d_ws + 2;
+  int* barcnt = (int*)d_ws + 4;
+  int* bargen = (int*)d_ws + 5;
   float* wsf = (float*)d_ws;
   float* F2   = wsf + 16;
   float* rA   = F2 + 393216;
@@ -670,7 +743,7 @@
   bf16* Fp1   = (bf16*)(big + 1048576);
 
   k_detect<<<1, 256, 0, stream>>>((const unsigned short*)feats_l1, flag);
-  k_setone<<<1, 1, 0, stream>>>(oneflag);
+  k_zero2<<<1, 1, 0, stream>>>(barcnt, bargen);
   k_cvt<<<1, 256, 0, stream>>>(ref1_b1, cb1a, 128, flag);
   k_cvt<<<1, 256, 0, stream>>>(ref1_b2, cb1b, 2, flag);
   k_cvt<<<1, 256, 0, stream>>>(ref0_b1, cb0a, 64, flag);
@@ -684,54 +757,15 @@
   k_trans_feats<<<384, 256, 0, stream>>>(feats_l1, Fp1, 3, 64, 4096, flag);
 
   k_corr<<<dim3(1024, 2), 64, 0, stream>>>(Fp2, corrTb);
-  k_gemm_w<64, 4, 0, false, 1, 0, 0><<<dim3(3, 128), 64, 0, stream>>>(
-      corrTb, wtok, 0, tok_b, 192, flag, nullptr, x, 192, oneflag,
-      nullptr, nullptr, nullptr, nullptr, 0, nullptr, 0);
-
-  auto run_block = [&](const void* ln1w, long o1, const void* ln1b, long o2,
-                       const void* inw, long o3, const void* inb, long o4,
-                       const void* ow, long o5, const void* ob, long o6,
-                       const void* ln2w, long o7, const void* ln2b, long o8,
-                       const void* w1, long o9, const void* b1, long o10,
-                       const void* w2, long o11, const void* b2, long o12) {
-    k_gemm_w<192, 4, 0, false, 3, 1, 1><<<dim3(9, 128), 64, 0, stream>>>(
-        x, inw, o3, inb, o4, flag, nullptr, qkvbb, 576, flag,
-        nullptr, nullptr, vtb, ln1w, o1, ln1b, o2);
-    k_attn_mfma<<<dim3(64, 4, 2), 256, 0, stream>>>(qkvbb, vtb, opart, mlbuf);
-    k_gemm_w<192, 4, 0, true, 2, 0, 0><<<dim3(3, 128), 64, 0, stream>>>(
-        nullptr, ow, o5, ob, o6, flag, x, x, 192, flag,
-        opart, mlbuf, nullptr, nullptr, 0, nullptr, 0);
-    k_gemm_w<192, 4, 1, false, 3, 1, 0><<<dim3(12, 128), 64, 0, stream>>>(
-        x, w1, o9, b1, o10, flag, nullptr, hidb, 768, flag,
-        nullptr, nullptr, nullptr, ln2w, o7, ln2b, o8);
-    k_gemm_w<768, 4, 0, true, 1, 0, 0><<<dim3(3, 128), 64, 0, stream>>>(
-        hidb, w2, o11, b2, o12, flag, x, x, 192, flag,
-        nullptr, nullptr, nullptr, nullptr, 0, nullptr, 0);
-  };
-
-  for (int i = 0; i < 6; ++i) {
-    run_block(lcm_ln1_w, (long)i * 192, lcm_ln1_b, (long)i * 192,
-              lcm_in_w, (long)i * 110592, lcm_in_b, (long)i * 576,
-              lcm_out_w, (long)i * 36864, lcm_out_b, (long)i * 192,
-              lcm_ln2_w, (long)i * 192, lcm_ln2_b, (long)i * 192,
-              lcm_mlp_w1, (long)i * 147456, lcm_mlp_b1, (long)i * 768,
-              lcm_mlp_w2, (long)i * 147456, lcm_mlp_b2, (long)i * 192);
-  }
-  k_ema<<<768, 256, 0, stream>>>(x);
-
-  for (int i = 0; i < 2; ++i) {
-    run_block(gtr_ln1_w, (long)i * 192, gtr_ln1_b, (long)i * 192,
-              gtr_in_w, (long)i * 110592, gtr_in_b, (long)i * 576,
-              gtr_out_w, (long)i * 36864, gtr_out_b, (long)i * 192,
-              gtr_ln2_w, (long)i * 192, gtr_ln2_b, (long)i * 192,
-              gtr_mlp_w1, (long)i * 147456, gtr_mlp_b1, (long)i * 768,
-              gtr_mlp_w2, (long)i * 147456, gtr_mlp_b2, (long)i * 192);
-  }
-
-  k_gemm_w<192, 4, 1, false, 0, 0, 0><<<dim3(3, 128), 64, 0, stream>>>(
-      x, head_w1, 0, head_b1, 0, flag, nullptr, headh, 192, flag,
-      nullptr, nullptr, nullptr, nullptr, 0, nullptr, 0);
-  k_head2<<<1024, 256, 0, stream>>>(headh, head_w2, head_b2, cur, flag);
+
+  k_mega<<<256, 256, 0, stream>>>(
+      flag, barcnt, bargen, x, corrTb, wtok, tok_b,
+      qkvbb, vtb, opart, mlbuf, hidb, headh, cur,
+      lcm_ln1_w, lcm_ln1_b, lcm_in_w, lcm_in_b, lcm_out_w, lcm_out_b,
+      lcm_ln2_w, lcm_ln2_b, lcm_mlp_w1, lcm_mlp_b1, lcm_mlp_w2, lcm_mlp_b2,
+      gtr_ln1_w, gtr_ln1_b, gtr_in_w, gtr_in_b, gtr_out_w, gtr_out_b,
+      gtr_ln2_w, gtr_ln2_b, gtr_mlp_w1, gtr_mlp_b1, gtr_mlp_w2, gtr_mlp_b2,
+      head_w1, head_b1, head_w2, head_b2);
 
   k_zerosh<<<768, 256, 0, stream>>>((unsigned short*)rT, 196608);
 
```

Measured after the change: 3.560 ms. +253.4%, slower.
